# Optimization experiments

Hardware: AMD Instinct MI355X
Metric: run time of the kernel (lower is better)

## Reference

```python
import jax, jax.numpy as jnp
import numpy as np

B, N_ATOMS, N_ALIGN = 65536, 128, 64


def setup_inputs() -> dict:
    key = jax.random.key(0)
    k1, k2 = jax.random.split(key)
    traj = jax.random.normal(k1, (B, N_ATOMS, 3), dtype=jnp.float32)
    ref_pos = jax.random.normal(k2, (N_ATOMS, 3), dtype=jnp.float32)
    align_idx = jnp.arange(N_ALIGN, dtype=jnp.int32)  # 0-based (ids - 1)
    return {"traj": traj, "ref_pos": ref_pos, "align_idx": align_idx}


def reference(traj, ref_pos, align_idx):
    # --- __init__: centered reference coordinates of alignment atoms ---
    ref_x = ref_pos[align_idx]                      # [K, 3]
    ref_x = ref_x - jnp.mean(ref_x, axis=0)         # center

    # --- forward: Kabsch alignment per frame ---
    sel = traj[:, align_idx, :]                     # [B, K, 3]
    x_c = jnp.mean(sel, axis=1, keepdims=True)      # [B, 1, 3]
    x_notran = sel - x_c                            # [B, K, 3]
    # xtmp = x_notran^T  -> prod[b] = x_notran[b]^T @ ref_x : [B, 3, 3]
    prod = jnp.einsum('bki,kj->bij', x_notran, ref_x)

    u, s, vh = jnp.linalg.svd(prod)                 # u,vh: [B, 3, 3]
    sign_vec = jnp.sign(jnp.linalg.det(u @ vh))     # [B]
    # diag(1, 1, sign) applied on the right of u
    d = jnp.stack([jnp.ones_like(sign_vec), jnp.ones_like(sign_vec), sign_vec], axis=-1)
    rotate_mat = (u * d[:, None, :]) @ vh           # [B, 3, 3]

    aligned_traj = jnp.matmul(traj - x_c, rotate_mat)  # [B, N, 3]
    return aligned_traj
```

## Files before the change

### kernel.cpp

```cpp
#include <hip/hip_runtime.h>
#include <math.h>

#define NATOMS 128
#define NALIGN 64
#define FPB    32
#define TPF    16
#define TPB    (FPB * TPF)

#define JACOBI_ROT(app, aqq, apq, arp, arq, pcol, qcol)                 \
  {                                                                     \
    float _apq = (apq);                                                 \
    float _den = 2.0f * _apq;                                           \
    _den = copysignf(fmaxf(fabsf(_den), 1e-30f), _den);                 \
    float _tau = ((aqq) - (app)) / _den;                                \
    float _t = (_tau >= 0.0f ? 1.0f : -1.0f) /                          \
               (fabsf(_tau) + sqrtf(1.0f + _tau * _tau));               \
    float _c = rsqrtf(1.0f + _t * _t);                                  \
    float _s = _t * _c;                                                 \
    (app) -= _t * _apq;                                                 \
    (aqq) += _t * _apq;                                                 \
    (apq) = 0.0f;                                                       \
    float _rp = (arp), _rq = (arq);                                     \
    (arp) = _c * _rp - _s * _rq;                                        \
    (arq) = _s * _rp + _c * _rq;                                        \
    _Pragma("unroll")                                                   \
    for (int _r = 0; _r < 3; _r++) {                                    \
      float _vp = v[3 * _r + (pcol)], _vq = v[3 * _r + (qcol)];         \
      v[3 * _r + (pcol)] = _c * _vp - _s * _vq;                         \
      v[3 * _r + (qcol)] = _s * _vp + _c * _vq;                         \
    }                                                                   \
  }

__global__ __launch_bounds__(TPB) void align_kernel(
    const float* __restrict__ traj,
    const float* __restrict__ ref_pos,
    const int* __restrict__ align_idx,
    float* __restrict__ out,
    int B)
{
    __shared__ float4 s_rmap[NATOMS];
    __shared__ float s_cov[FPB][13];

    const int t   = threadIdx.x;
    const int f   = t >> 4;
    const int sub = t & 15;
    const int gf  = blockIdx.x * FPB + f;
    const bool valid = (gf < B);

    float x[8], y[8], z[8];
    if (valid) {
        const float4* p = (const float4*)(traj + (size_t)gf * (NATOMS * 3) + sub * 24);
        float4 q0 = p[0], q1 = p[1], q2 = p[2], q3 = p[3], q4 = p[4], q5 = p[5];
        x[0]=q0.x; y[0]=q0.y; z[0]=q0.z;
        x[1]=q0.w; y[1]=q1.x; z[1]=q1.y;
        x[2]=q1.z; y[2]=q1.w; z[2]=q2.x;
        x[3]=q2.y; y[3]=q2.z; z[3]=q2.w;
        x[4]=q3.x; y[4]=q3.y; z[4]=q3.z;
        x[5]=q3.w; y[5]=q4.x; z[5]=q4.y;
        x[6]=q4.z; y[6]=q4.w; z[6]=q5.x;
        x[7]=q5.y; y[7]=q5.z; z[7]=q5.w;
    } else {
        #pragma unroll
        for (int j = 0; j < 8; j++) { x[j]=0.f; y[j]=0.f; z[j]=0.f; }
    }

    if (t < NALIGN) {
        const float4 z4 = make_float4(0.f, 0.f, 0.f, 0.f);
        s_rmap[t]          = z4;
        s_rmap[t + NALIGN] = z4;

        int idx = align_idx[t];
        float rx = ref_pos[idx * 3 + 0];
        float ry = ref_pos[idx * 3 + 1];
        float rz = ref_pos[idx * 3 + 2];
        float sx = rx, sy = ry, sz = rz;
        #pragma unroll
        for (int off = 32; off >= 1; off >>= 1) {
            sx += __shfl_xor(sx, off);
            sy += __shfl_xor(sy, off);
            sz += __shfl_xor(sz, off);
        }
        const float inv = 1.0f / (float)NALIGN;
        int slot = ((idx & 7) << 4) | (idx >> 3);
        s_rmap[slot] = make_float4(rx - sx * inv, ry - sy * inv, rz - sz * inv, 1.0f);
    }
    __syncthreads();

    {
        float sx = 0.f, sy = 0.f, sz = 0.f;
        float c[9] = {0.f,0.f,0.f,0.f,0.f,0.f,0.f,0.f,0.f};
        #pragma unroll
        for (int j = 0; j < 8; j++) {
            float4 rm = s_rmap[(j << 4) | sub];
            sx += rm.w * x[j]; sy += rm.w * y[j]; sz += rm.w * z[j];
            c[0] += x[j]*rm.x; c[1] += x[j]*rm.y; c[2] += x[j]*rm.z;
            c[3] += y[j]*rm.x; c[4] += y[j]*rm.y; c[5] += y[j]*rm.z;
            c[6] += z[j]*rm.x; c[7] += z[j]*rm.y; c[8] += z[j]*rm.z;
        }
        #pragma unroll
        for (int off = 8; off >= 1; off >>= 1) {
            sx += __shfl_xor(sx, off);
            sy += __shfl_xor(sy, off);
            sz += __shfl_xor(sz, off);
            #pragma unroll
            for (int jj = 0; jj < 9; jj++) c[jj] += __shfl_xor(c[jj], off);
        }
        if (sub == 0) {
            #pragma unroll
            for (int jj = 0; jj < 9; jj++) s_cov[f][jj] = c[jj];
            const float inv = 1.0f / (float)NALIGN;
            s_cov[f][9]  = sx * inv;
            s_cov[f][10] = sy * inv;
            s_cov[f][11] = sz * inv;
        }
    }
    __syncthreads();

    if (t < FPB) {
        float m[9];
        #pragma unroll
        for (int j = 0; j < 9; j++) m[j] = s_cov[t][j];

        float a00 = m[0]*m[0] + m[3]*m[3] + m[6]*m[6];
        float a01 = m[0]*m[1] + m[3]*m[4] + m[6]*m[7];
        float a02 = m[0]*m[2] + m[3]*m[5] + m[6]*m[8];
        float a11 = m[1]*m[1] + m[4]*m[4] + m[7]*m[7];
        float a12 = m[1]*m[2] + m[4]*m[5] + m[7]*m[8];
        float a22 = m[2]*m[2] + m[5]*m[5] + m[8]*m[8];

        float v[9] = {1.f,0.f,0.f, 0.f,1.f,0.f, 0.f,0.f,1.f};
        #pragma unroll
        for (int sweep = 0; sweep < 5; sweep++) {
            JACOBI_ROT(a00, a11, a01, a02, a12, 0, 1);
            JACOBI_ROT(a00, a22, a02, a01, a12, 0, 2);
            JACOBI_ROT(a11, a22, a12, a01, a02, 1, 2);
        }

        float dd[3] = {a00, a11, a22};
        #pragma unroll
        for (int pass = 0; pass < 3; pass++) {
            const int ii = (pass == 2) ? 1 : 0;
            const int jj = (pass == 0) ? 1 : 2;
            float di = dd[ii], dj = dd[jj];
            bool sw = di < dj;
            dd[ii] = sw ? dj : di;
            dd[jj] = sw ? di : dj;
            #pragma unroll
            for (int rr = 0; rr < 3; rr++) {
                float a = v[3*rr+ii], b = v[3*rr+jj];
                v[3*rr+ii] = sw ? b : a;
                v[3*rr+jj] = sw ? a : b;
            }
        }

        float v0x = v[0], v0y = v[3], v0z = v[6];
        float v1x = v[1], v1y = v[4], v1z = v[7];
        float v2x = v[2], v2y = v[5], v2z = v[8];

        float u1x = m[0]*v0x + m[1]*v0y + m[2]*v0z;
        float u1y = m[3]*v0x + m[4]*v0y + m[5]*v0z;
        float u1z = m[6]*v0x + m[7]*v0y + m[8]*v0z;
        float n1 = rsqrtf(fmaxf(u1x*u1x + u1y*u1y + u1z*u1z, 1e-30f));
        u1x *= n1; u1y *= n1; u1z *= n1;

        float u2x = m[0]*v1x + m[1]*v1y + m[2]*v1z;
        float u2y = m[3]*v1x + m[4]*v1y + m[5]*v1z;
        float u2z = m[6]*v1x + m[7]*v1y + m[8]*v1z;
        float d12 = u1x*u2x + u1y*u2y + u1z*u2z;
        u2x -= d12 * u1x; u2y -= d12 * u1y; u2z -= d12 * u1z;
        float n2 = rsqrtf(fmaxf(u2x*u2x + u2y*u2y + u2z*u2z, 1e-30f));
        u2x *= n2; u2y *= n2; u2z *= n2;

        float u3x = u1y*u2z - u1z*u2y;
        float u3y = u1z*u2x - u1x*u2z;
        float u3z = u1x*u2y - u1y*u2x;
        float cxv = v1y*v2z - v1z*v2y;
        float cyv = v1z*v2x - v1x*v2z;
        float czv = v1x*v2y - v1y*v2x;
        float detv = v0x*cxv + v0y*cyv + v0z*czv;
        float sg = (detv >= 0.f) ? 1.f : -1.f;
        u3x *= sg; u3y *= sg; u3z *= sg;

        s_cov[t][0] = u1x*v0x + u2x*v1x + u3x*v2x;
        s_cov[t][1] = u1x*v0y + u2x*v1y + u3x*v2y;
        s_cov[t][2] = u1x*v0z + u2x*v1z + u3x*v2z;
        s_cov[t][3] = u1y*v0x + u2y*v1x + u3y*v2x;
        s_cov[t][4] = u1y*v0y + u2y*v1y + u3y*v2y;
        s_cov[t][5] = u1y*v0z + u2y*v1z + u3y*v2z;
        s_cov[t][6] = u1z*v0x + u2z*v1x + u3z*v2x;
        s_cov[t][7] = u1z*v0y + u2z*v1y + u3z*v2y;
        s_cov[t][8] = u1z*v0z + u2z*v1z + u3z*v2z;
    }
    __syncthreads();

    if (valid) {
        float R0 = s_cov[f][0], R1 = s_cov[f][1], R2 = s_cov[f][2];
        float R3 = s_cov[f][3], R4 = s_cov[f][4], R5 = s_cov[f][5];
        float R6 = s_cov[f][6], R7 = s_cov[f][7], R8 = s_cov[f][8];
        float xcx = s_cov[f][9], xcy = s_cov[f][10], xcz = s_cov[f][11];

        float ox[8], oy[8], oz[8];
        #pragma unroll
        for (int j = 0; j < 8; j++) {
            float dx = x[j] - xcx, dy = y[j] - xcy, dz = z[j] - xcz;
            ox[j] = dx*R0 + dy*R3 + dz*R6;
            oy[j] = dx*R1 + dy*R4 + dz*R7;
            oz[j] = dx*R2 + dy*R5 + dz*R8;
        }

        float4* po = (float4*)(out + (size_t)gf * (NATOMS * 3) + sub * 24);
        po[0] = make_float4(ox[0], oy[0], oz[0], ox[1]);
        po[1] = make_float4(oy[1], oz[1], ox[2], oy[2]);
        po[2] = make_float4(oz[2], ox[3], oy[3], oz[3]);
        po[3] = make_float4(ox[4], oy[4], oz[4], ox[5]);
        po[4] = make_float4(oy[5], oz[5], ox[6], oy[6]);
        po[5] = make_float4(oz[6], ox[7], oy[7], oz[7]);
    }
}

extern "C" void kernel_launch(void* const* d_in, const int* in_sizes, int n_in,
                              void* d_out, int out_size, void* d_ws, size_t ws_size,
                              hipStream_t stream) {
    const float* traj      = (const float*)d_in[0];
    const float* ref_pos   = (const float*)d_in[1];
    const int*   align_idx = (const int*)d_in[2];
    float*       out       = (float*)d_out;

    int B = in_sizes[0] / (NATOMS * 3);
    int grid = (B + FPB - 1) / FPB;
    align_kernel<<<grid, TPB, 0, stream>>>(traj, ref_pos, align_idx, out, B);
}
```

Before: 198.3 us.

## Split alignment into covariance/SVD kernel and separate apply kernel via workspace

```diff
diff --git a/kernel.cpp b/kernel.cpp
--- a/kernel.cpp
+++ b/kernel.cpp
@@ -3,9 +3,10 @@
 
 #define NATOMS 128
 #define NALIGN 64
-#define FPB    32
-#define TPF    16
-#define TPB    (FPB * TPF)
+
+#define TPB1   256
+#define FPB1   16
+#define TPB2   256
 
 #define JACOBI_ROT(app, aqq, apq, arp, arq, pcol, qcol)                 \
   {                                                                     \
@@ -31,20 +32,93 @@
     }                                                                   \
   }
 
-__global__ __launch_bounds__(TPB) void align_kernel(
+__device__ __forceinline__ void svd_rotation(const float* m, float* R)
+{
+    float a00 = m[0]*m[0] + m[3]*m[3] + m[6]*m[6];
+    float a01 = m[0]*m[1] + m[3]*m[4] + m[6]*m[7];
+    float a02 = m[0]*m[2] + m[3]*m[5] + m[6]*m[8];
+    float a11 = m[1]*m[1] + m[4]*m[4] + m[7]*m[7];
+    float a12 = m[1]*m[2] + m[4]*m[5] + m[7]*m[8];
+    float a22 = m[2]*m[2] + m[5]*m[5] + m[8]*m[8];
+
+    float v[9] = {1.f,0.f,0.f, 0.f,1.f,0.f, 0.f,0.f,1.f};
+    #pragma unroll
+    for (int sweep = 0; sweep < 5; sweep++) {
+        JACOBI_ROT(a00, a11, a01, a02, a12, 0, 1);
+        JACOBI_ROT(a00, a22, a02, a01, a12, 0, 2);
+        JACOBI_ROT(a11, a22, a12, a01, a02, 1, 2);
+    }
+
+    float dd[3] = {a00, a11, a22};
+    #pragma unroll
+    for (int pass = 0; pass < 3; pass++) {
+        const int ii = (pass == 2) ? 1 : 0;
+        const int jj = (pass == 0) ? 1 : 2;
+        float di = dd[ii], dj = dd[jj];
+        bool sw = di < dj;
+        dd[ii] = sw ? dj : di;
+        dd[jj] = sw ? di : dj;
+        #pragma unroll
+        for (int rr = 0; rr < 3; rr++) {
+            float a = v[3*rr+ii], b = v[3*rr+jj];
+            v[3*rr+ii] = sw ? b : a;
+            v[3*rr+jj] = sw ? a : b;
+        }
+    }
+
+    float v0x = v[0], v0y = v[3], v0z = v[6];
+    float v1x = v[1], v1y = v[4], v1z = v[7];
+    float v2x = v[2], v2y = v[5], v2z = v[8];
+
+    float u1x = m[0]*v0x + m[1]*v0y + m[2]*v0z;
+    float u1y = m[3]*v0x + m[4]*v0y + m[5]*v0z;
+    float u1z = m[6]*v0x + m[7]*v0y + m[8]*v0z;
+    float n1 = rsqrtf(fmaxf(u1x*u1x + u1y*u1y + u1z*u1z, 1e-30f));
+    u1x *= n1; u1y *= n1; u1z *= n1;
+
+    float u2x = m[0]*v1x + m[1]*v1y + m[2]*v1z;
+    float u2y = m[3]*v1x + m[4]*v1y + m[5]*v1z;
+    float u2z = m[6]*v1x + m[7]*v1y + m[8]*v1z;
+    float d12 = u1x*u2x + u1y*u2y + u1z*u2z;
+    u2x -= d12 * u1x; u2y -= d12 * u1y; u2z -= d12 * u1z;
+    float n2 = rsqrtf(fmaxf(u2x*u2x + u2y*u2y + u2z*u2z, 1e-30f));
+    u2x *= n2; u2y *= n2; u2z *= n2;
+
+    float u3x = u1y*u2z - u1z*u2y;
+    float u3y = u1z*u2x - u1x*u2z;
+    float u3z = u1x*u2y - u1y*u2x;
+    float cxv = v1y*v2z - v1z*v2y;
+    float cyv = v1z*v2x - v1x*v2z;
+    float czv = v1x*v2y - v1y*v2x;
+    float detv = v0x*cxv + v0y*cyv + v0z*czv;
+    float sg = (detv >= 0.f) ? 1.f : -1.f;
+    u3x *= sg; u3y *= sg; u3z *= sg;
+
+    R[0] = u1x*v0x + u2x*v1x + u3x*v2x;
+    R[1] = u1x*v0y + u2x*v1y + u3x*v2y;
+    R[2] = u1x*v0z + u2x*v1z + u3x*v2z;
+    R[3] = u1y*v0x + u2y*v1x + u3y*v2x;
+    R[4] = u1y*v0y + u2y*v1y + u3y*v2y;
+    R[5] = u1y*v0z + u2y*v1z + u3y*v2z;
+    R[6] = u1z*v0x + u2z*v1x + u3z*v2x;
+    R[7] = u1z*v0y + u2z*v1y + u3z*v2y;
+    R[8] = u1z*v0z + u2z*v1z + u3z*v2z;
+}
+
+__global__ __launch_bounds__(TPB1) void cov_svd_kernel(
     const float* __restrict__ traj,
     const float* __restrict__ ref_pos,
     const int* __restrict__ align_idx,
-    float* __restrict__ out,
+    float* __restrict__ rmat,
     int B)
 {
     __shared__ float4 s_rmap[NATOMS];
-    __shared__ float s_cov[FPB][13];
+    __shared__ float  s_cov[FPB1][13];
 
     const int t   = threadIdx.x;
     const int f   = t >> 4;
     const int sub = t & 15;
-    const int gf  = blockIdx.x * FPB + f;
+    const int gf  = blockIdx.x * FPB1 + f;
     const bool valid = (gf < B);
 
     float x[8], y[8], z[8];
@@ -116,80 +190,162 @@
     }
     __syncthreads();
 
-    if (t < FPB) {
+    if (t < FPB1) {
+        int g = blockIdx.x * FPB1 + t;
+        if (g < B) {
+            float m[9];
+            #pragma unroll
+            for (int j = 0; j < 9; j++) m[j] = s_cov[t][j];
+            float R[9];
+            svd_rotation(m, R);
+            float4* dst = (float4*)(rmat + (size_t)g * 12);
+            dst[0] = make_float4(R[0], R[1], R[2], R[3]);
+            dst[1] = make_float4(R[4], R[5], R[6], R[7]);
+            dst[2] = make_float4(R[8], s_cov[t][9], s_cov[t][10], s_cov[t][11]);
+        }
+    }
+}
+
+__global__ __launch_bounds__(TPB2) void apply_kernel(
+    const float* __restrict__ traj,
+    const float* __restrict__ rmat,
+    float* __restrict__ out,
+    int B)
+{
+    const int gidx = blockIdx.x * TPB2 + threadIdx.x;
+    const int f    = gidx >> 4;
+    const int sub  = gidx & 15;
+    if (f >= B) return;
+
+    const float4* p = (const float4*)(traj + (size_t)f * (NATOMS * 3) + sub * 24);
+    float4 q0 = p[0], q1 = p[1], q2 = p[2], q3 = p[3], q4 = p[4], q5 = p[5];
+
+    const float4* Rt = (const float4*)(rmat + (size_t)f * 12);
+    float4 Ra = Rt[0], Rb = Rt[1], Rc = Rt[2];
+    float R0 = Ra.x, R1 = Ra.y, R2 = Ra.z, R3 = Ra.w;
+    float R4 = Rb.x, R5 = Rb.y, R6 = Rb.z, R7 = Rb.w;
+    float R8 = Rc.x, xcx = Rc.y, xcy = Rc.z, xcz = Rc.w;
+
+    float x[8], y[8], z[8];
+    x[0]=q0.x; y[0]=q0.y; z[0]=q0.z;
+    x[1]=q0.w; y[1]=q1.x; z[1]=q1.y;
+    x[2]=q1.z; y[2]=q1.w; z[2]=q2.x;
+    x[3]=q2.y; y[3]=q2.z; z[3]=q2.w;
+    x[4]=q3.x; y[4]=q3.y; z[4]=q3.z;
+    x[5]=q3.w; y[5]=q4.x; z[5]=q4.y;
+    x[6]=q4.z; y[6]=q4.w; z[6]=q5.x;
+    x[7]=q5.y; y[7]=q5.z; z[7]=q5.w;
+
+    float ox[8], oy[8], oz[8];
+    #pragma unroll
+    for (int j = 0; j < 8; j++) {
+        float dx = x[j] - xcx, dy = y[j] - xcy, dz = z[j] - xcz;
+        ox[j] = dx*R0 + dy*R3 + dz*R6;
+        oy[j] = dx*R1 + dy*R4 + dz*R7;
+        oz[j] = dx*R2 + dy*R5 + dz*R8;
+    }
+
+    float4* po = (float4*)(out + (size_t)f * (NATOMS * 3) + sub * 24);
+    po[0] = make_float4(ox[0], oy[0], oz[0], ox[1]);
+    po[1] = make_float4(oy[1], oz[1], ox[2], oy[2]);
+    po[2] = make_float4(oz[2], ox[3], oy[3], oz[3]);
+    po[3] = make_float4(ox[4], oy[4], oz[4], ox[5]);
+    po[4] = make_float4(oy[5], oz[5], ox[6], oy[6]);
+    po[5] = make_float4(oz[6], ox[7], oy[7], oz[7]);
+}
+
+__global__ __launch_bounds__(512) void align_fused_kernel(
+    const float* __restrict__ traj,
+    const float* __restrict__ ref_pos,
+    const int* __restrict__ align_idx,
+    float* __restrict__ out,
+    int B)
+{
+    __shared__ float4 s_rmap[NATOMS];
+    __shared__ float s_cov[32][13];
+
+    const int t   = threadIdx.x;
+    const int f   = t >> 4;
+    const int sub = t & 15;
+    const int gf  = blockIdx.x * 32 + f;
+    const bool valid = (gf < B);
+
+    float x[8], y[8], z[8];
+    if (valid) {
+        const float4* p = (const float4*)(traj + (size_t)gf * (NATOMS * 3) + sub * 24);
+        float4 q0 = p[0], q1 = p[1], q2 = p[2], q3 = p[3], q4 = p[4], q5 = p[5];
+        x[0]=q0.x; y[0]=q0.y; z[0]=q0.z;
+        x[1]=q0.w; y[1]=q1.x; z[1]=q1.y;
+        x[2]=q1.z; y[2]=q1.w; z[2]=q2.x;
+        x[3]=q2.y; y[3]=q2.z; z[3]=q2.w;
+        x[4]=q3.x; y[4]=q3.y; z[4]=q3.z;
+        x[5]=q3.w; y[5]=q4.x; z[5]=q4.y;
+        x[6]=q4.z; y[6]=q4.w; z[6]=q5.x;
+        x[7]=q5.y; y[7]=q5.z; z[7]=q5.w;
+    } else {
+        #pragma unroll
+        for (int j = 0; j < 8; j++) { x[j]=0.f; y[j]=0.f; z[j]=0.f; }
+    }
+
+    if (t < NALIGN) {
+        const float4 z4 = make_float4(0.f, 0.f, 0.f, 0.f);
+        s_rmap[t]          = z4;
+        s_rmap[t + NALIGN] = z4;
+        int idx = align_idx[t];
+        float rx = ref_pos[idx * 3 + 0];
+        float ry = ref_pos[idx * 3 + 1];
+        float rz = ref_pos[idx * 3 + 2];
+        float sx = rx, sy = ry, sz = rz;
+        #pragma unroll
+        for (int off = 32; off >= 1; off >>= 1) {
+            sx += __shfl_xor(sx, off);
+            sy += __shfl_xor(sy, off);
+            sz += __shfl_xor(sz, off);
+        }
+        const float inv = 1.0f / (float)NALIGN;
+        int slot = ((idx & 7) << 4) | (idx >> 3);
+        s_rmap[slot] = make_float4(rx - sx * inv, ry - sy * inv, rz - sz * inv, 1.0f);
+    }
+    __syncthreads();
+
+    {
+        float sx = 0.f, sy = 0.f, sz = 0.f;
+        float c[9] = {0.f,0.f,0.f,0.f,0.f,0.f,0.f,0.f,0.f};
+        #pragma unroll
+        for (int j = 0; j < 8; j++) {
+            float4 rm = s_rmap[(j << 4) | sub];
+            sx += rm.w * x[j]; sy += rm.w * y[j]; sz += rm.w * z[j];
+            c[0] += x[j]*rm.x; c[1] += x[j]*rm.y; c[2] += x[j]*rm.z;
+            c[3] += y[j]*rm.x; c[4] += y[j]*rm.y; c[5] += y[j]*rm.z;
+            c[6] += z[j]*rm.x; c[7] += z[j]*rm.y; c[8] += z[j]*rm.z;
+        }
+        #pragma unroll
+        for (int off = 8; off >= 1; off >>= 1) {
+            sx += __shfl_xor(sx, off);
+            sy += __shfl_xor(sy, off);
+            sz += __shfl_xor(sz, off);
+            #pragma unroll
+            for (int jj = 0; jj < 9; jj++) c[jj] += __shfl_xor(c[jj], off);
+        }
+        if (sub == 0) {
+            #pragma unroll
+            for (int jj = 0; jj < 9; jj++) s_cov[f][jj] = c[jj];
+            const float inv = 1.0f / (float)NALIGN;
+            s_cov[f][9]  = sx * inv;
+            s_cov[f][10] = sy * inv;
+            s_cov[f][11] = sz * inv;
+        }
+    }
+    __syncthreads();
+
+    if (t < 32) {
         float m[9];
         #pragma unroll
         for (int j = 0; j < 9; j++) m[j] = s_cov[t][j];
-
-        float a00 = m[0]*m[0] + m[3]*m[3] + m[6]*m[6];
-        float a01 = m[0]*m[1] + m[3]*m[4] + m[6]*m[7];
-        float a02 = m[0]*m[2] + m[3]*m[5] + m[6]*m[8];
-        float a11 = m[1]*m[1] + m[4]*m[4] + m[7]*m[7];
-        float a12 = m[1]*m[2] + m[4]*m[5] + m[7]*m[8];
-        float a22 = m[2]*m[2] + m[5]*m[5] + m[8]*m[8];
-
-        float v[9] = {1.f,0.f,0.f, 0.f,1.f,0.f, 0.f,0.f,1.f};
-        #pragma unroll
-        for (int sweep = 0; sweep < 5; sweep++) {
-            JACOBI_ROT(a00, a11, a01, a02, a12, 0, 1);
-            JACOBI_ROT(a00, a22, a02, a01, a12, 0, 2);
-            JACOBI_ROT(a11, a22, a12, a01, a02, 1, 2);
-        }
-
-        float dd[3] = {a00, a11, a22};
-        #pragma unroll
-        for (int pass = 0; pass < 3; pass++) {
-            const int ii = (pass == 2) ? 1 : 0;
-            const int jj = (pass == 0) ? 1 : 2;
-            float di = dd[ii], dj = dd[jj];
-            bool sw = di < dj;
-            dd[ii] = sw ? dj : di;
-            dd[jj] = sw ? di : dj;
-            #pragma unroll
-            for (int rr = 0; rr < 3; rr++) {
-                float a = v[3*rr+ii], b = v[3*rr+jj];
-                v[3*rr+ii] = sw ? b : a;
-                v[3*rr+jj] = sw ? a : b;
-            }
-        }
-
-        float v0x = v[0], v0y = v[3], v0z = v[6];
-        float v1x = v[1], v1y = v[4], v1z = v[7];
-        float v2x = v[2], v2y = v[5], v2z = v[8];
-
-        float u1x = m[0]*v0x + m[1]*v0y + m[2]*v0z;
-        float u1y = m[3]*v0x + m[4]*v0y + m[5]*v0z;
-        float u1z = m[6]*v0x + m[7]*v0y + m[8]*v0z;
-        float n1 = rsqrtf(fmaxf(u1x*u1x + u1y*u1y + u1z*u1z, 1e-30f));
-        u1x *= n1; u1y *= n1; u1z *= n1;
-
-        float u2x = m[0]*v1x + m[1]*v1y + m[2]*v1z;
-        float u2y = m[3]*v1x + m[4]*v1y + m[5]*v1z;
-        float u2z = m[6]*v1x + m[7]*v1y + m[8]*v1z;
-        float d12 = u1x*u2x + u1y*u2y + u1z*u2z;
-        u2x -= d12 * u1x; u2y -= d12 * u1y; u2z -= d12 * u1z;
-        float n2 = rsqrtf(fmaxf(u2x*u2x + u2y*u2y + u2z*u2z, 1e-30f));
-        u2x *= n2; u2y *= n2; u2z *= n2;
-
-        float u3x = u1y*u2z - u1z*u2y;
-        float u3y = u1z*u2x - u1x*u2z;
-        float u3z = u1x*u2y - u1y*u2x;
-        float cxv = v1y*v2z - v1z*v2y;
-        float cyv = v1z*v2x - v1x*v2z;
-        float czv = v1x*v2y - v1y*v2x;
-        float detv = v0x*cxv + v0y*cyv + v0z*czv;
-        float sg = (detv >= 0.f) ? 1.f : -1.f;
-        u3x *= sg; u3y *= sg; u3z *= sg;
-
-        s_cov[t][0] = u1x*v0x + u2x*v1x + u3x*v2x;
-        s_cov[t][1] = u1x*v0y + u2x*v1y + u3x*v2y;
-        s_cov[t][2] = u1x*v0z + u2x*v1z + u3x*v2z;
-        s_cov[t][3] = u1y*v0x + u2y*v1x + u3y*v2x;
-        s_cov[t][4] = u1y*v0y + u2y*v1y + u3y*v2y;
-        s_cov[t][5] = u1y*v0z + u2y*v1z + u3y*v2z;
-        s_cov[t][6] = u1z*v0x + u2z*v1x + u3z*v2x;
-        s_cov[t][7] = u1z*v0y + u2z*v1y + u3z*v2y;
-        s_cov[t][8] = u1z*v0z + u2z*v1z + u3z*v2z;
+        float R[9];
+        svd_rotation(m, R);
+        #pragma unroll
+        for (int j = 0; j < 9; j++) s_cov[t][j] = R[j];
     }
     __syncthreads();
 
@@ -207,7 +363,6 @@
             oy[j] = dx*R1 + dy*R4 + dz*R7;
             oz[j] = dx*R2 + dy*R5 + dz*R8;
         }
-
         float4* po = (float4*)(out + (size_t)gf * (NATOMS * 3) + sub * 24);
         po[0] = make_float4(ox[0], oy[0], oz[0], ox[1]);
         po[1] = make_float4(oy[1], oz[1], ox[2], oy[2]);
@@ -227,6 +382,17 @@
     float*       out       = (float*)d_out;
 
     int B = in_sizes[0] / (NATOMS * 3);
-    int grid = (B + FPB - 1) / FPB;
-    align_kernel<<<grid, TPB, 0, stream>>>(traj, ref_pos, align_idx, out, B);
-}
+    size_t need = (size_t)B * 12 * sizeof(float);
+
+    if (d_ws != nullptr && ws_size >= need) {
+        float* rmat = (float*)d_ws;
+        int grid1 = (B + FPB1 - 1) / FPB1;
+        cov_svd_kernel<<<grid1, TPB1, 0, stream>>>(traj, ref_pos, align_idx, rmat, B);
+        long long threads2 = (long long)B * 16;
+        int grid2 = (int)((threads2 + TPB2 - 1) / TPB2);
+        apply_kernel<<<grid2, TPB2, 0, stream>>>(traj, rmat, out, B);
+    } else {
+        int grid = (B + 31) / 32;
+        align_fused_kernel<<<grid, 512, 0, stream>>>(traj, ref_pos, align_idx, out, B);
+    }
+}
```

Result: slower. 209.8 us (+5.8%).
